# Kernel tuning notes

Measured on AMD Instinct MI355X. Metric: run time of the kernel, lower is better.

The kernel has to match this reference:

```python
import jax, jax.numpy as jnp
import numpy as np

H = 64  # rnn_size == input_size
CANVAS = 25


def _init_params(key, vocab_size):
    ks = jax.random.split(key, 14)
    s = 0.05
    p = {}
    p['embed'] = jax.random.normal(ks[0], (vocab_size + 1, H), jnp.float32) * s
    p['W_ih'] = jax.random.normal(ks[1], (4 * H, H), jnp.float32) * s
    p['W_hh'] = jax.random.normal(ks[2], (4 * H, H), jnp.float32) * s
    p['b_ih'] = jax.random.normal(ks[3], (4 * H,), jnp.float32) * s
    p['b_hh'] = jax.random.normal(ks[4], (4 * H,), jnp.float32) * s
    p['Wc'] = jax.random.normal(ks[5], (3, H), jnp.float32) * s
    p['bc'] = jax.random.normal(ks[6], (3,), jnp.float32) * s
    p['Ws'] = jax.random.normal(ks[7], (3, H), jnp.float32) * s
    p['bs'] = jax.random.normal(ks[8], (3,), jnp.float32) * s
    p['Wo'] = jax.random.normal(ks[9], (2, H), jnp.float32) * s
    p['bo'] = jax.random.normal(ks[10], (2,), jnp.float32) * s
    p['Wr1'] = jax.random.normal(ks[11], (32, H + 1 + 4), jnp.float32) * s
    p['br1'] = jnp.zeros((32,), jnp.float32)
    p['Wr2'] = jax.random.normal(ks[12], (1, 32), jnp.float32) * s
    p['br2'] = jnp.zeros((1,), jnp.float32)
    return p


def setup_inputs() -> dict:
    key = jax.random.key(0)
    k1, k2, k3, k4, k5 = jax.random.split(key, 5)
    B, T, V = 4096, 128, 32000
    inp = {
        'inst': jax.random.randint(k1, (B, T), 0, V, dtype=jnp.int64)
        if jax.config.jax_enable_x64 else jax.random.randint(k1, (B, T), 0, V, dtype=jnp.int32),
        'prev_canvas': jax.random.normal(k2, (B, CANVAS, 4), jnp.float32),
        'ref_obj': jax.random.normal(k3, (B, 4), jnp.float32),
        'target_obj': jax.random.normal(k4, (B, 4), jnp.float32),
    }
    inp.update(_init_params(k5, V))
    return inp


def _encode(inst, embed, W_ih, W_hh, b_ih, b_hh):
    # inst: [B, T] -> h: [B, H] via sequential LSTMCell
    xs = embed[inst]                       # [B, T, H]
    xs = jnp.swapaxes(xs, 0, 1)            # [T, B, H]
    B = inst.shape[0]
    h0 = jnp.zeros((B, H), xs.dtype)
    c0 = jnp.zeros((B, H), xs.dtype)

    def step(carry, x):
        h, c = carry
        gates = x @ W_ih.T + b_ih + h @ W_hh.T + b_hh   # [B, 4H]
        i, f, g, o = jnp.split(gates, 4, axis=-1)
        i, f, o = jax.nn.sigmoid(i), jax.nn.sigmoid(f), jax.nn.sigmoid(o)
        c = f * c + i * jnp.tanh(g)
        h = o * jnp.tanh(c)
        return (h, c), None

    (h, _), _ = jax.lax.scan(step, (h0, c0), xs)
    return h


def _act_tag(inst):
    # 1.0 if last token with value >= 1 equals 9, else 0.0
    T = inst.shape[1]
    mask = inst >= 1                                   # [B, T]
    last_pos = T - 1 - jnp.argmax(mask[:, ::-1], axis=1)
    last_val = jnp.take_along_axis(inst, last_pos[:, None], axis=1)[:, 0]
    tag = jnp.where((last_val == 9) & mask.any(axis=1), 1.0, 0.0)
    return tag.astype(jnp.float32)


def reference(inst, prev_canvas, ref_obj, target_obj, embed, W_ih, W_hh, b_ih, b_hh,
              Wc, bc, Ws, bs, Wo, bo, Wr1, br1, Wr2, br2):
    h = _encode(inst, embed, W_ih, W_hh, b_ih, b_hh)           # [B, H]
    tag = _act_tag(inst)                                       # [B]
    inst2 = jnp.concatenate([h, tag[:, None]], axis=1)         # [B, H+1]
    inst2 = jnp.broadcast_to(inst2[:, None, :], (h.shape[0], CANVAS, H + 1))
    feat = jnp.concatenate([inst2, prev_canvas], axis=2)       # [B, 25, 69]
    hid = jax.nn.relu(jnp.einsum('bnf,of->bno', feat, Wr1) + br1)
    score = (jnp.einsum('bno,ro->bnr', hid, Wr2) + br2)[..., 0]  # [B, 25]
    weight = jax.nn.softmax(score, axis=1)
    ref_pred = jnp.einsum('bn,bnd->bd', weight, prev_canvas)   # [B, 4]
    offset = jnp.clip(h @ Wo.T + bo, -1.0, 1.0)                # hardtanh, [B, 2]
    color_out = jax.nn.log_softmax(h @ Wc.T + bc, axis=1)      # [B, 3]
    shape_out = jax.nn.log_softmax(h @ Ws.T + bs, axis=1)      # [B, 3]
    row_out = ref_pred[:, 2] + offset[:, 0]
    col_out = ref_pred[:, 3] + offset[:, 1]
    return (color_out, shape_out, row_out, col_out)
```

## Files before the change

### kernel.cpp

```cpp
#include <hip/hip_runtime.h>
#include <hip/hip_bf16.h>

#define HH 64
#define TT 128
#define BT 16

typedef __attribute__((ext_vector_type(8))) short bf16x8;
typedef __attribute__((ext_vector_type(4))) float f32x4;

__device__ __forceinline__ unsigned short f2bf(float f) {
  union { float f; unsigned u; } v; v.f = f;
  return (unsigned short)((v.u + 0x7FFFu + ((v.u >> 16) & 1u)) >> 16);
}
__device__ __forceinline__ float rcp_(float x) { return __builtin_amdgcn_rcpf(x); }
__device__ __forceinline__ float exp2_(float x) { return __builtin_amdgcn_exp2f(x); }

#define L2E 1.44269504f
#define L2E2 2.88539008f

__device__ __forceinline__ float red32(float v) {
#pragma unroll
  for (int s = 16; s; s >>= 1) v += __shfl_xor(v, s, 32);
  return v;
}

__global__ void convert_embed(const float* __restrict__ src,
                              unsigned short* __restrict__ dst, int n) {
  int base = (blockIdx.x * 256 + threadIdx.x) * 4;
  if (base + 4 <= n) {
    float4 v = *(const float4*)(src + base);
    ushort4 r;
    r.x = f2bf(v.x); r.y = f2bf(v.y); r.z = f2bf(v.z); r.w = f2bf(v.w);
    *(ushort4*)(dst + base) = r;
  } else {
    for (int k = base; k < n; k++) dst[k] = f2bf(src[k]);
  }
}

#define MFMA(acc, a, b) acc = __builtin_amdgcn_mfma_f32_16x16x32_bf16(a, b, acc, 0, 0, 0)

__global__ __launch_bounds__(512, 1) void lstm_k(
    const int* __restrict__ inst, const unsigned short* __restrict__ ebf,
    const float* __restrict__ Wih, const float* __restrict__ Whh,
    const float* __restrict__ bih, const float* __restrict__ bhh,
    const float* __restrict__ canvas,
    const float* __restrict__ Wc, const float* __restrict__ bc,
    const float* __restrict__ Ws, const float* __restrict__ bs,
    const float* __restrict__ Wo, const float* __restrict__ bo,
    const float* __restrict__ Wr1, const float* __restrict__ br1,
    const float* __restrict__ Wr2, const float* __restrict__ br2,
    float* __restrict__ out, int B)
{
  __shared__ int tokT[TT * BT];
  __shared__ unsigned short hsh[2 * BT * HH];
  __shared__ float a_s[16][66];
  __shared__ float Wr1_s[32 * 69];

  const int tid  = threadIdx.x;
  const int lane = tid & 63;
  const int w    = tid >> 6;
  const int wid  = w & 3;
  const int hi   = w >> 2;
  const int fr   = lane & 15;
  const int fg   = lane >> 4;
  const int b0   = blockIdx.x * BT;
  const int jcol = wid * 16 + fr;
  const int n0   = hi * 64 + jcol;
  const int n1   = n0 + 128;

  for (int i = tid; i < BT * TT; i += 512)
    tokT[(i & (TT - 1)) * BT + (i >> 7)] = inst[b0 * TT + i];
  for (int i = tid; i < BT * HH; i += 512) hsh[i] = 0;
  for (int i = tid; i < 32 * 69; i += 512) Wr1_s[i] = Wr1[i];

  bf16x8 wt[2][2][2];
  float nb0, sb1;
#pragma unroll
  for (int tile = 0; tile < 2; tile++) {
    const int n = tile ? n1 : n0;
#pragma unroll
    for (int kt = 0; kt < 2; kt++) {
      const float* pa = Wih + n * 64 + kt * 32 + fg * 8;
      const float* pb = Whh + n * 64 + kt * 32 + fg * 8;
      bf16x8 fa, fb;
#pragma unroll
      for (int j = 0; j < 8; j++) { fa[j] = (short)f2bf(pa[j]); fb[j] = (short)f2bf(pb[j]); }
      wt[tile][kt][0] = fa; wt[tile][kt][1] = fb;
    }
  }
  nb0 = -L2E * (bih[n0] + bhh[n0]);
  sb1 = (hi ? -L2E : L2E2) * (bih[n1] + bhh[n1]);

  bf16x8 xa0, xa1;
  {
    const int tk = tokT[0 * BT + fr];
    const unsigned short* p = ebf + tk * 64 + fg * 8;
    xa0 = *(const bf16x8*)p; xa1 = *(const bf16x8*)(p + 32);
  }
  f32x4 Dx0 = {0.f,0.f,0.f,0.f}, Dx1 = {0.f,0.f,0.f,0.f};
  MFMA(Dx0, xa0, wt[0][0][0]); MFMA(Dx0, xa1, wt[0][1][0]);
  MFMA(Dx1, xa0, wt[1][0][0]); MFMA(Dx1, xa1, wt[1][1][0]);
  {
    const int tk = tokT[1 * BT + fr];
    const unsigned short* p = ebf + tk * 64 + fg * 8;
    xa0 = *(const bf16x8*)p; xa1 = *(const bf16x8*)(p + 32);
  }

  float cst[4] = {0.f,0.f,0.f,0.f};
  float pf[4], po[4];

  __syncthreads();

  for (int t = 0; t < TT; t++) {
    const char* hb = (const char*)hsh + (t & 1) * (BT * HH * 2);
    const int sx = (fr & 7) << 4;
    bf16x8 ha0 = *(const bf16x8*)(hb + ((fr * 128 + fg * 16) ^ sx));
    bf16x8 ha1 = *(const bf16x8*)(hb + ((fr * 128 + 64 + fg * 16) ^ sx));

    f32x4 D0 = Dx0, D1 = Dx1;
    MFMA(D0, ha0, wt[0][0][1]); MFMA(D0, ha1, wt[0][1][1]);
    MFMA(D1, ha0, wt[1][0][1]); MFMA(D1, ha1, wt[1][1][1]);

    if (hi == 0) {
#pragma unroll
      for (int r = 0; r < 4; r++) {
        const int m = fg * 4 + r;
        const float gi = rcp_(1.f + exp2_(fmaf(D0[r], -L2E, nb0)));
        const float e  = exp2_(fmaf(D1[r], L2E2, sb1));
        const float tg = (e - 1.f) * rcp_(e + 1.f);
        a_s[m][jcol] = gi * tg;
      }
    } else {
#pragma unroll
      for (int r = 0; r < 4; r++) {
        pf[r] = rcp_(1.f + exp2_(fmaf(D0[r], -L2E, nb0)));
        po[r] = rcp_(1.f + exp2_(fmaf(D1[r], -L2E, sb1)));
      }
    }
    __syncthreads();

    if (t + 1 < TT) {
      f32x4 nx0 = {0.f,0.f,0.f,0.f}, nx1 = {0.f,0.f,0.f,0.f};
      MFMA(nx0, xa0, wt[0][0][0]); MFMA(nx0, xa1, wt[0][1][0]);
      MFMA(nx1, xa0, wt[1][0][0]); MFMA(nx1, xa1, wt[1][1][0]);
      Dx0 = nx0; Dx1 = nx1;
      if (t + 2 < TT) {
        const int tk = tokT[(t + 2) * BT + fr];
        const unsigned short* p = ebf + tk * 64 + fg * 8;
        xa0 = *(const bf16x8*)p; xa1 = *(const bf16x8*)(p + 32);
      }
    }
    if (hi == 1) {
      char* hwb = (char*)hsh + ((t + 1) & 1) * (BT * HH * 2);
#pragma unroll
      for (int r = 0; r < 4; r++) {
        const int m = fg * 4 + r;
        const float a = a_s[m][jcol];
        const float c = fmaf(pf[r], cst[r], a);
        cst[r] = c;
        const float e  = exp2_(L2E2 * fminf(c, 15.f));
        const float th = (e - 1.f) * rcp_(e + 1.f);
        const float hn = po[r] * th;
        *(unsigned short*)(hwb + ((m * 128 + 2 * jcol) ^ ((m & 7) << 4))) = f2bf(hn);
        if (t == TT - 1) a_s[m][jcol] = hn;
      }
    }
    __syncthreads();
  }

  const int m  = (w << 1) + (lane >> 5);
  const int o  = lane & 31;
  const int gb = b0 + m;

  int key = -1;
#pragma unroll
  for (int q = 0; q < 4; q++) {
    const int t = o + q * 32;
    const int tk = tokT[t * BT + m];
    if (tk >= 1) key = max(key, (t << 16) | tk);
  }
#pragma unroll
  for (int s = 16; s; s >>= 1) key = max(key, __shfl_xor(key, s, 32));
  const float tag = (key >= 0 && (key & 0xFFFF) == 9) ? 1.f : 0.f;

  float base = br1[o] + Wr1_s[o * 69 + 64] * tag;
  for (int f = 0; f < 64; f++) base += Wr1_s[o * 69 + f] * a_s[m][f];
  const float wr2o = Wr2[o];
  const float* cv = canvas + (size_t)gb * 100;

  float sc[25];
  float mx = -1e30f;
#pragma unroll
  for (int n = 0; n < 25; n++) {
    float acc = base;
#pragma unroll
    for (int d = 0; d < 4; d++) acc += Wr1_s[o * 69 + 65 + d] * cv[n * 4 + d];
    float p = wr2o * fmaxf(acc, 0.f);
#pragma unroll
    for (int s = 16; s; s >>= 1) p += __shfl_xor(p, s, 32);
    sc[n] = p + br2[0];
    mx = fmaxf(mx, sc[n]);
  }
  float sum = 0.f, rp2 = 0.f, rp3 = 0.f;
#pragma unroll
  for (int n = 0; n < 25; n++) {
    const float e = __expf(sc[n] - mx);
    sum += e;
    rp2 += e * cv[n * 4 + 2];
    rp3 += e * cv[n * 4 + 3];
  }
  const float inv = 1.f / sum;

  const float h0 = a_s[m][o], h1 = a_s[m][o + 32];
  float c0 = red32(h0 * Wc[o]       + h1 * Wc[32 + o]) + bc[0];
  float c1 = red32(h0 * Wc[64 + o]  + h1 * Wc[96 + o]) + bc[1];
  float c2 = red32(h0 * Wc[128 + o] + h1 * Wc[160 + o]) + bc[2];
  float s0 = red32(h0 * Ws[o]       + h1 * Ws[32 + o]) + bs[0];
  float s1 = red32(h0 * Ws[64 + o]  + h1 * Ws[96 + o]) + bs[1];
  float s2 = red32(h0 * Ws[128 + o] + h1 * Ws[160 + o]) + bs[2];
  float o0 = red32(h0 * Wo[o]       + h1 * Wo[32 + o]) + bo[0];
  float o1 = red32(h0 * Wo[64 + o]  + h1 * Wo[96 + o]) + bo[1];
  o0 = fminf(fmaxf(o0, -1.f), 1.f);
  o1 = fminf(fmaxf(o1, -1.f), 1.f);

  const float cm = fmaxf(c0, fmaxf(c1, c2));
  const float cl = cm + __logf(__expf(c0 - cm) + __expf(c1 - cm) + __expf(c2 - cm));
  const float sm = fmaxf(s0, fmaxf(s1, s2));
  const float sl = sm + __logf(__expf(s0 - sm) + __expf(s1 - sm) + __expf(s2 - sm));

  if (o == 0) {
    out[gb * 3 + 0] = c0 - cl; out[gb * 3 + 1] = c1 - cl; out[gb * 3 + 2] = c2 - cl;
    float* shp = out + (size_t)3 * B;
    shp[gb * 3 + 0] = s0 - sl; shp[gb * 3 + 1] = s1 - sl; shp[gb * 3 + 2] = s2 - sl;
    out[(size_t)6 * B + gb] = rp2 * inv + o0;
    out[(size_t)7 * B + gb] = rp3 * inv + o1;
  }
}

extern "C" void kernel_launch(void* const* d_in, const int* in_sizes, int n_in,
                              void* d_out, int out_size, void* d_ws, size_t ws_size,
                              hipStream_t stream) {
  const int*   inst   = (const int*)  d_in[0];
  const float* canvas = (const float*)d_in[1];
  const float* embed  = (const float*)d_in[4];
  const float* Wih    = (const float*)d_in[5];
  const float* Whh    = (const float*)d_in[6];
  const float* bih    = (const float*)d_in[7];
  const float* bhh    = (const float*)d_in[8];
  const float* Wc     = (const float*)d_in[9];
  const float* bc     = (const float*)d_in[10];
  const float* Ws_    = (const float*)d_in[11];
  const float* bs     = (const float*)d_in[12];
  const float* Wo     = (const float*)d_in[13];
  const float* bo     = (const float*)d_in[14];
  const float* Wr1    = (const float*)d_in[15];
  const float* br1    = (const float*)d_in[16];
  const float* Wr2    = (const float*)d_in[17];
  const float* br2    = (const float*)d_in[18];

  const int B  = in_sizes[0] / TT;
  const int NE = in_sizes[4];

  unsigned short* ebf = (unsigned short*)d_ws;

  convert_embed<<<(NE / 4 + 255) / 256, 256, 0, stream>>>(embed, ebf, NE);
  lstm_k<<<B / BT, 512, 0, stream>>>(inst, ebf, Wih, Whh, bih, bhh,
                                     canvas, Wc, bc, Ws_, bs, Wo, bo,
                                     Wr1, br1, Wr2, br2, (float*)d_out, B);
}
```

Before: 112.8 us.

## Halve batch tile, merge all four gates per wave, single barrier per step

```diff
diff --git a/kernel.cpp b/kernel.cpp
--- a/kernel.cpp
+++ b/kernel.cpp
@@ -3,7 +3,7 @@
 
 #define HH 64
 #define TT 128
-#define BT 16
+#define BT 8
 
 typedef __attribute__((ext_vector_type(8))) short bf16x8;
 typedef __attribute__((ext_vector_type(4))) float f32x4;
@@ -39,7 +39,7 @@
 
 #define MFMA(acc, a, b) acc = __builtin_amdgcn_mfma_f32_16x16x32_bf16(a, b, acc, 0, 0, 0)
 
-__global__ __launch_bounds__(512, 1) void lstm_k(
+__global__ __launch_bounds__(256, 2) void lstm_k(
     const int* __restrict__ inst, const unsigned short* __restrict__ ebf,
     const float* __restrict__ Wih, const float* __restrict__ Whh,
     const float* __restrict__ bih, const float* __restrict__ bhh,
@@ -53,31 +53,32 @@
 {
   __shared__ int tokT[TT * BT];
   __shared__ unsigned short hsh[2 * BT * HH];
-  __shared__ float a_s[16][66];
+  __shared__ float h_s[BT][HH + 2];
   __shared__ float Wr1_s[32 * 69];
+  __shared__ float cv_s[BT * 100];
 
   const int tid  = threadIdx.x;
   const int lane = tid & 63;
   const int w    = tid >> 6;
-  const int wid  = w & 3;
-  const int hi   = w >> 2;
   const int fr   = lane & 15;
   const int fg   = lane >> 4;
   const int b0   = blockIdx.x * BT;
-  const int jcol = wid * 16 + fr;
-  const int n0   = hi * 64 + jcol;
-  const int n1   = n0 + 128;
-
-  for (int i = tid; i < BT * TT; i += 512)
-    tokT[(i & (TT - 1)) * BT + (i >> 7)] = inst[b0 * TT + i];
-  for (int i = tid; i < BT * HH; i += 512) hsh[i] = 0;
-  for (int i = tid; i < 32 * 69; i += 512) Wr1_s[i] = Wr1[i];
-
-  bf16x8 wt[2][2][2];
-  float nb0, sb1;
-#pragma unroll
-  for (int tile = 0; tile < 2; tile++) {
-    const int n = tile ? n1 : n0;
+  const int jcol = w * 16 + fr;
+  const int hi2  = fg >> 1;
+  const int row0 = (fg & 1) * 4 + hi2 * 2;
+
+  for (int i = tid; i < BT * TT; i += 256) {
+    const int b = i >> 7, t = i & (TT - 1);
+    tokT[t * BT + b] = inst[(size_t)(b0 + b) * TT + t];
+  }
+  for (int i = tid; i < 2 * BT * HH; i += 256) hsh[i] = 0;
+  for (int i = tid; i < 32 * 69; i += 256) Wr1_s[i] = Wr1[i];
+  for (int i = tid; i < BT * 100; i += 256) cv_s[i] = canvas[(size_t)b0 * 100 + i];
+
+  bf16x8 wt[4][2][2];
+#pragma unroll
+  for (int q = 0; q < 4; q++) {
+    const int n = (w + q * 4) * 16 + fr;
 #pragma unroll
     for (int kt = 0; kt < 2; kt++) {
       const float* pa = Wih + n * 64 + kt * 32 + fg * 8;
@@ -85,91 +86,103 @@
       bf16x8 fa, fb;
 #pragma unroll
       for (int j = 0; j < 8; j++) { fa[j] = (short)f2bf(pa[j]); fb[j] = (short)f2bf(pb[j]); }
-      wt[tile][kt][0] = fa; wt[tile][kt][1] = fb;
+      wt[q][kt][0] = fa; wt[q][kt][1] = fb;
     }
   }
-  nb0 = -L2E * (bih[n0] + bhh[n0]);
-  sb1 = (hi ? -L2E : L2E2) * (bih[n1] + bhh[n1]);
+  const float nbi = -L2E  * (bih[jcol]       + bhh[jcol]);
+  const float nbf = -L2E  * (bih[64 + jcol]  + bhh[64 + jcol]);
+  const float sbg =  L2E2 * (bih[128 + jcol] + bhh[128 + jcol]);
+  const float nbo = -L2E  * (bih[192 + jcol] + bhh[192 + jcol]);
+
+  const int rr7 = fr & 7;
+  const int ra  = (rr7 * 128 + fg * 16) ^ (rr7 << 4);
+  const int rb  = (rr7 * 128 + 64 + fg * 16) ^ (rr7 << 4);
+  const int wa0 = (row0 * 128 + 2 * jcol) ^ ((row0 & 7) << 4);
+  const int wa1 = ((row0 + 1) * 128 + 2 * jcol) ^ (((row0 + 1) & 7) << 4);
+  char* const hs0 = (char*)hsh;
+  char* const hs1 = hs0 + BT * HH * 2;
+
+  __syncthreads();
 
   bf16x8 xa0, xa1;
   {
-    const int tk = tokT[0 * BT + fr];
+    const int tk = tokT[0 * BT + rr7];
     const unsigned short* p = ebf + tk * 64 + fg * 8;
     xa0 = *(const bf16x8*)p; xa1 = *(const bf16x8*)(p + 32);
   }
-  f32x4 Dx0 = {0.f,0.f,0.f,0.f}, Dx1 = {0.f,0.f,0.f,0.f};
-  MFMA(Dx0, xa0, wt[0][0][0]); MFMA(Dx0, xa1, wt[0][1][0]);
-  MFMA(Dx1, xa0, wt[1][0][0]); MFMA(Dx1, xa1, wt[1][1][0]);
-  {
-    const int tk = tokT[1 * BT + fr];
-    const unsigned short* p = ebf + tk * 64 + fg * 8;
-    xa0 = *(const bf16x8*)p; xa1 = *(const bf16x8*)(p + 32);
-  }
-
-  float cst[4] = {0.f,0.f,0.f,0.f};
-  float pf[4], po[4];
-
+  float cst0 = 0.f, cst1 = 0.f, hk0 = 0.f, hk1 = 0.f;
+
+#define LSTM_STEP(RD, WR, T)                                                   \
+  {                                                                            \
+    bf16x8 ha0 = *(const bf16x8*)(RD + ra);                                    \
+    bf16x8 ha1 = *(const bf16x8*)(RD + rb);                                    \
+    const int tn = ((T) + 1 < TT) ? (T) + 1 : TT - 1;                          \
+    const int tk = tokT[tn * BT + rr7];                                        \
+    const unsigned short* px = ebf + tk * 64 + fg * 8;                         \
+    bf16x8 xn0 = *(const bf16x8*)px;                                           \
+    bf16x8 xn1 = *(const bf16x8*)(px + 32);                                    \
+    f32x4 D0 = {0.f,0.f,0.f,0.f}, D1 = {0.f,0.f,0.f,0.f},                      \
+          D2 = {0.f,0.f,0.f,0.f}, D3 = {0.f,0.f,0.f,0.f};                      \
+    MFMA(D0, xa0, wt[0][0][0]); MFMA(D0, xa1, wt[0][1][0]);                    \
+    MFMA(D1, xa0, wt[1][0][0]); MFMA(D1, xa1, wt[1][1][0]);                    \
+    MFMA(D2, xa0, wt[2][0][0]); MFMA(D2, xa1, wt[2][1][0]);                    \
+    MFMA(D3, xa0, wt[3][0][0]); MFMA(D3, xa1, wt[3][1][0]);                    \
+    MFMA(D0, ha0, wt[0][0][1]); MFMA(D0, ha1, wt[0][1][1]);                    \
+    MFMA(D1, ha0, wt[1][0][1]); MFMA(D1, ha1, wt[1][1][1]);                    \
+    MFMA(D2, ha0, wt[2][0][1]); MFMA(D2, ha1, wt[2][1][1]);                    \
+    MFMA(D3, ha0, wt[3][0][1]); MFMA(D3, ha1, wt[3][1][1]);                    \
+    {                                                                          \
+      const float i_ = hi2 ? D0[2] : D0[0];                                    \
+      const float f_ = hi2 ? D1[2] : D1[0];                                    \
+      const float g_ = hi2 ? D2[2] : D2[0];                                    \
+      const float o_ = hi2 ? D3[2] : D3[0];                                    \
+      const float gi = rcp_(1.f + exp2_(fmaf(i_, -L2E, nbi)));                 \
+      const float gf = rcp_(1.f + exp2_(fmaf(f_, -L2E, nbf)));                 \
+      const float eg = exp2_(fminf(fmaf(g_, L2E2, sbg), 60.f));                \
+      const float tg = (eg - 1.f) * rcp_(eg + 1.f);                            \
+      const float go = rcp_(1.f + exp2_(fmaf(o_, -L2E, nbo)));                 \
+      const float c  = fmaf(gf, cst0, gi * tg);                                \
+      cst0 = c;                                                                \
+      const float ec = exp2_(L2E2 * fminf(c, 8.f));                            \
+      const float th = (ec - 1.f) * rcp_(ec + 1.f);                            \
+      hk0 = go * th;                                                           \
+      union { float f; unsigned u; } cv; cv.f = hk0;                           \
+      *(unsigned short*)(WR + wa0) = (unsigned short)((cv.u + 0x8000u) >> 16); \
+    }                                                                          \
+    {                                                                          \
+      const float i_ = hi2 ? D0[3] : D0[1];                                    \
+      const float f_ = hi2 ? D1[3] : D1[1];                                    \
+      const float g_ = hi2 ? D2[3] : D2[1];                                    \
+      const float o_ = hi2 ? D3[3] : D3[1];                                    \
+      const float gi = rcp_(1.f + exp2_(fmaf(i_, -L2E, nbi)));                 \
+      const float gf = rcp_(1.f + exp2_(fmaf(f_, -L2E, nbf)));                 \
+      const float eg = exp2_(fminf(fmaf(g_, L2E2, sbg), 60.f));                \
+      const float tg = (eg - 1.f) * rcp_(eg + 1.f);                            \
+      const float go = rcp_(1.f + exp2_(fmaf(o_, -L2E, nbo)));                 \
+      const float c  = fmaf(gf, cst1, gi * tg);                                \
+      cst1 = c;                                                                \
+      const float ec = exp2_(L2E2 * fminf(c, 8.f));                            \
+      const float th = (ec - 1.f) * rcp_(ec + 1.f);                            \
+      hk1 = go * th;                                                           \
+      union { float f; unsigned u; } cv; cv.f = hk1;                           \
+      *(unsigned short*)(WR + wa1) = (unsigned short)((cv.u + 0x8000u) >> 16); \
+    }                                                                          \
+    __syncthreads();                                                           \
+    xa0 = xn0; xa1 = xn1;                                                      \
+  }
+
+  for (int t = 0; t < TT; t += 2) {
+    LSTM_STEP(hs0, hs1, t);
+    LSTM_STEP(hs1, hs0, t + 1);
+  }
+#undef LSTM_STEP
+
+  h_s[row0][jcol]     = hk0;
+  h_s[row0 + 1][jcol] = hk1;
   __syncthreads();
 
-  for (int t = 0; t < TT; t++) {
-    const char* hb = (const char*)hsh + (t & 1) * (BT * HH * 2);
-    const int sx = (fr & 7) << 4;
-    bf16x8 ha0 = *(const bf16x8*)(hb + ((fr * 128 + fg * 16) ^ sx));
-    bf16x8 ha1 = *(const bf16x8*)(hb + ((fr * 128 + 64 + fg * 16) ^ sx));
-
-    f32x4 D0 = Dx0, D1 = Dx1;
-    MFMA(D0, ha0, wt[0][0][1]); MFMA(D0, ha1, wt[0][1][1]);
-    MFMA(D1, ha0, wt[1][0][1]); MFMA(D1, ha1, wt[1][1][1]);
-
-    if (hi == 0) {
-#pragma unroll
-      for (int r = 0; r < 4; r++) {
-        const int m = fg * 4 + r;
-        const float gi = rcp_(1.f + exp2_(fmaf(D0[r], -L2E, nb0)));
-        const float e  = exp2_(fmaf(D1[r], L2E2, sb1));
-        const float tg = (e - 1.f) * rcp_(e + 1.f);
-        a_s[m][jcol] = gi * tg;
-      }
-    } else {
-#pragma unroll
-      for (int r = 0; r < 4; r++) {
-        pf[r] = rcp_(1.f + exp2_(fmaf(D0[r], -L2E, nb0)));
-        po[r] = rcp_(1.f + exp2_(fmaf(D1[r], -L2E, sb1)));
-      }
-    }
-    __syncthreads();
-
-    if (t + 1 < TT) {
-      f32x4 nx0 = {0.f,0.f,0.f,0.f}, nx1 = {0.f,0.f,0.f,0.f};
-      MFMA(nx0, xa0, wt[0][0][0]); MFMA(nx0, xa1, wt[0][1][0]);
-      MFMA(nx1, xa0, wt[1][0][0]); MFMA(nx1, xa1, wt[1][1][0]);
-      Dx0 = nx0; Dx1 = nx1;
-      if (t + 2 < TT) {
-        const int tk = tokT[(t + 2) * BT + fr];
-        const unsigned short* p = ebf + tk * 64 + fg * 8;
-        xa0 = *(const bf16x8*)p; xa1 = *(const bf16x8*)(p + 32);
-      }
-    }
-    if (hi == 1) {
-      char* hwb = (char*)hsh + ((t + 1) & 1) * (BT * HH * 2);
-#pragma unroll
-      for (int r = 0; r < 4; r++) {
-        const int m = fg * 4 + r;
-        const float a = a_s[m][jcol];
-        const float c = fmaf(pf[r], cst[r], a);
-        cst[r] = c;
-        const float e  = exp2_(L2E2 * fminf(c, 15.f));
-        const float th = (e - 1.f) * rcp_(e + 1.f);
-        const float hn = po[r] * th;
-        *(unsigned short*)(hwb + ((m * 128 + 2 * jcol) ^ ((m & 7) << 4))) = f2bf(hn);
-        if (t == TT - 1) a_s[m][jcol] = hn;
-      }
-    }
-    __syncthreads();
-  }
-
-  const int m  = (w << 1) + (lane >> 5);
-  const int o  = lane & 31;
+  const int m  = tid >> 5;
+  const int o  = tid & 31;
   const int gb = b0 + m;
 
   int key = -1;
@@ -184,9 +197,9 @@
   const float tag = (key >= 0 && (key & 0xFFFF) == 9) ? 1.f : 0.f;
 
   float base = br1[o] + Wr1_s[o * 69 + 64] * tag;
-  for (int f = 0; f < 64; f++) base += Wr1_s[o * 69 + f] * a_s[m][f];
+  for (int f = 0; f < 64; f++) base += Wr1_s[o * 69 + f] * h_s[m][f];
   const float wr2o = Wr2[o];
-  const float* cv = canvas + (size_t)gb * 100;
+  const float* cv = cv_s + m * 100;
 
   float sc[25];
   float mx = -1e30f;
@@ -211,15 +224,15 @@
   }
   const float inv = 1.f / sum;
 
-  const float h0 = a_s[m][o], h1 = a_s[m][o + 32];
-  float c0 = red32(h0 * Wc[o]       + h1 * Wc[32 + o]) + bc[0];
-  float c1 = red32(h0 * Wc[64 + o]  + h1 * Wc[96 + o]) + bc[1];
+  const float h0 = h_s[m][o], h1 = h_s[m][o + 32];
+  float c0 = red32(h0 * Wc[o]       + h1 * Wc[32 + o])  + bc[0];
+  float c1 = red32(h0 * Wc[64 + o]  + h1 * Wc[96 + o])  + bc[1];
   float c2 = red32(h0 * Wc[128 + o] + h1 * Wc[160 + o]) + bc[2];
-  float s0 = red32(h0 * Ws[o]       + h1 * Ws[32 + o]) + bs[0];
-  float s1 = red32(h0 * Ws[64 + o]  + h1 * Ws[96 + o]) + bs[1];
+  float s0 = red32(h0 * Ws[o]       + h1 * Ws[32 + o])  + bs[0];
+  float s1 = red32(h0 * Ws[64 + o]  + h1 * Ws[96 + o])  + bs[1];
   float s2 = red32(h0 * Ws[128 + o] + h1 * Ws[160 + o]) + bs[2];
-  float o0 = red32(h0 * Wo[o]       + h1 * Wo[32 + o]) + bo[0];
-  float o1 = red32(h0 * Wo[64 + o]  + h1 * Wo[96 + o]) + bo[1];
+  float o0 = red32(h0 * Wo[o]       + h1 * Wo[32 + o])  + bo[0];
+  float o1 = red32(h0 * Wo[64 + o]  + h1 * Wo[96 + o])  + bo[1];
   o0 = fminf(fmaxf(o0, -1.f), 1.f);
   o1 = fminf(fmaxf(o1, -1.f), 1.f);
 
@@ -264,7 +277,7 @@
   unsigned short* ebf = (unsigned short*)d_ws;
 
   convert_embed<<<(NE / 4 + 255) / 256, 256, 0, stream>>>(embed, ebf, NE);
-  lstm_k<<<B / BT, 512, 0, stream>>>(inst, ebf, Wih, Whh, bih, bhh,
+  lstm_k<<<B / BT, 256, 0, stream>>>(inst, ebf, Wih, Whh, bih, bhh,
                                      canvas, Wc, bc, Ws_, bs, Wo, bo,
                                      Wr1, br1, Wr2, br2, (float*)d_out, B);
 }
```

New measurement: 107.7 us. -4.5%, faster.
